# Performance work log

Hardware: AMD Instinct MI355X
Metric: run time of the kernel (lower is better)

Reference implementation:

```python
import jax, jax.numpy as jnp
import numpy as np

H = 16
D_MODEL = 1024
D_K = D_MODEL // H
NWORDS = 16384


def setup_inputs() -> dict:
    key0 = jax.random.key(0)
    ks = jax.random.split(key0, 11)
    s = 0.02
    return {
        "query": jax.random.normal(ks[0], (1, D_MODEL), dtype=jnp.float32),
        "key": jax.random.normal(ks[1], (NWORDS, D_MODEL), dtype=jnp.float32),
        "value": jax.random.normal(ks[2], (NWORDS, D_MODEL), dtype=jnp.float32),
        "Wq": jax.random.normal(ks[3], (D_MODEL, D_MODEL), dtype=jnp.float32) * s,
        "bq": jax.random.normal(ks[4], (D_MODEL,), dtype=jnp.float32) * s,
        "Wk": jax.random.normal(ks[5], (D_MODEL, D_MODEL), dtype=jnp.float32) * s,
        "bk": jax.random.normal(ks[6], (D_MODEL,), dtype=jnp.float32) * s,
        "Wv": jax.random.normal(ks[7], (D_MODEL, D_MODEL), dtype=jnp.float32) * s,
        "bv": jax.random.normal(ks[8], (D_MODEL,), dtype=jnp.float32) * s,
        "Wo": jax.random.normal(ks[9], (D_MODEL, D_MODEL), dtype=jnp.float32) * s,
        "bo": jax.random.normal(ks[10], (D_MODEL,), dtype=jnp.float32) * s,
    }


def reference(query, key, value, Wq, bq, Wk, bk, Wv, bv, Wo, bo):
    # torch Linear: y = x @ W.T + b
    q = (query @ Wq.T + bq).reshape(H, D_K)          # [h, d_k]  (single query token)
    k = (key @ Wk.T + bk).reshape(-1, H, D_K)        # [n, h, d_k]
    v = (value @ Wv.T + bv).reshape(-1, H, D_K)      # [n, h, d_k]
    # NOTE: original module applies NO 1/sqrt(d_k) scaling.
    scores = jnp.einsum("hd,nhd->hn", q, k)          # [h, n]
    p_attn = jax.nn.softmax(scores, axis=-1)          # dropout p=0 -> no-op
    x = jnp.einsum("hn,nhd->hd", p_attn, v).reshape(1, H * D_K)  # [1, d_model]
    return x @ Wo.T + bo                              # [1, d_model]
```

## Files before the change

kernel.cpp:

```cpp
#include <hip/hip_runtime.h>

#define DM 1024
#define NW 16384

#define OFF_C    1024
#define OFF_D0   17408
#define OFF_S    17424
#define OFF_X    17696
#define OFF_W    18720
#define OFF_E    36864
#define OFF_PART 299008

__global__ __launch_bounds__(256) void k_rowdot(const float* __restrict__ W,
                                                const float* __restrict__ v,
                                                const float* __restrict__ b,
                                                float* __restrict__ out) {
  const int wave = (blockIdx.x * 256 + threadIdx.x) >> 6;
  const int lane = threadIdx.x & 63;
  const float* row = W + (size_t)wave * DM + 4 * lane;
  float s = 0.f;
#pragma unroll
  for (int j = 0; j < 4; ++j) {
    float4 a = *(const float4*)(row + j * 256);
    float4 x = *(const float4*)(v + j * 256 + 4 * lane);
    s += a.x * x.x + a.y * x.y + a.z * x.z + a.w * x.w;
  }
#pragma unroll
  for (int off = 32; off; off >>= 1) s += __shfl_xor(s, off, 64);
  if (lane == 0) out[wave] = s + b[wave];
}

__global__ __launch_bounds__(256) void k_qck(const float* __restrict__ Wq,
                                             const float* __restrict__ bq,
                                             const float* __restrict__ query,
                                             const float* __restrict__ Wk,
                                             const float* __restrict__ bk,
                                             float* __restrict__ c,
                                             float* __restrict__ d0,
                                             float* __restrict__ S) {
  const int h = blockIdx.x >> 2;
  const int mc = blockIdx.x & 3;
  const int t = threadIdx.x;
  const int lane = t & 63;
  const int wv = t >> 6;
  __shared__ float qh[64];
  if (blockIdx.x == 0 && t < 16) S[t * 16] = 0.f;
  float4 qv[4];
#pragma unroll
  for (int j = 0; j < 4; ++j) qv[j] = *(const float4*)(query + j * 256 + 4 * lane);
#pragma unroll 1
  for (int i = 0; i < 16; i += 2) {
    const int d0i = 4 * i + wv;
    const int d1i = 4 * (i + 1) + wv;
    const float* r0 = Wq + (size_t)(h * 64 + d0i) * DM + 4 * lane;
    const float* r1 = Wq + (size_t)(h * 64 + d1i) * DM + 4 * lane;
    float4 a0[4], a1[4];
#pragma unroll
    for (int j = 0; j < 4; ++j) { a0[j] = *(const float4*)(r0 + j * 256);
                                  a1[j] = *(const float4*)(r1 + j * 256); }
    float s0 = 0.f, s1 = 0.f;
#pragma unroll
    for (int j = 0; j < 4; ++j) {
      s0 += a0[j].x * qv[j].x + a0[j].y * qv[j].y + a0[j].z * qv[j].z + a0[j].w * qv[j].w;
      s1 += a1[j].x * qv[j].x + a1[j].y * qv[j].y + a1[j].z * qv[j].z + a1[j].w * qv[j].w;
    }
#pragma unroll
    for (int off = 32; off; off >>= 1) { s0 += __shfl_xor(s0, off, 64);
                                         s1 += __shfl_xor(s1, off, 64); }
    if (lane == 0) { qh[d0i] = s0 + bq[h * 64 + d0i];
                     qh[d1i] = s1 + bq[h * 64 + d1i]; }
  }
  __syncthreads();
  const int m = mc * 256 + t;
  const float* Wp = Wk + (size_t)(h * 64) * DM + m;
  float s = 0.f;
#pragma unroll 1
  for (int db = 0; db < 8; ++db) {
    float wv8[8];
#pragma unroll
    for (int j = 0; j < 8; ++j) wv8[j] = Wp[(size_t)(db * 8 + j) * DM];
#pragma unroll
    for (int j = 0; j < 8; ++j) s = fmaf(qh[db * 8 + j], wv8[j], s);
  }
  c[h * DM + m] = s;
  if (mc == 0 && t == 0) {
    float tt = 0.f;
    for (int d = 0; d < 64; ++d) tt += qh[d] * bk[h * 64 + d];
    d0[h] = tt;
  }
}

__global__ __launch_bounds__(256, 3) void k_scores(const float* __restrict__ key,
                                                   const float* __restrict__ c,
                                                   const float* __restrict__ d0,
                                                   float* __restrict__ e,
                                                   float* __restrict__ S) {
  const int lane = threadIdx.x & 63;
  const int wv = threadIdx.x >> 6;
  const int hbase = wv * 4;
  const int n0 = blockIdx.x * 16;
  float4 cf[4][4];
#pragma unroll
  for (int hh = 0; hh < 4; ++hh)
#pragma unroll
    for (int j = 0; j < 4; ++j)
      cf[hh][j] = *(const float4*)(c + (size_t)(hbase + hh) * DM + j * 256 + 4 * lane);
  const int hl = (lane >> 4) & 3;
  const float dh = d0[hbase + hl];
  const bool hi5 = (lane & 32) != 0;
  const bool hi4 = (lane & 16) != 0;
  const bool writer = (lane & 15) == 0;
  float Ssum = 0.f;
  const float* kbase = key + (size_t)n0 * DM + 4 * lane;
  float4 kb[2][4];
#pragma unroll
  for (int j = 0; j < 4; ++j) {
    kb[0][j] = *(const float4*)(kbase + j * 256);
    kb[1][j] = *(const float4*)(kbase + DM + j * 256);
  }
#pragma unroll
  for (int rr = 0; rr < 8; ++rr) {
    float4 kn[2][4];
    if (rr < 7) {
      const float* kp = kbase + (size_t)(2 * rr + 2) * DM;
#pragma unroll
      for (int j = 0; j < 4; ++j) {
        kn[0][j] = *(const float4*)(kp + j * 256);
        kn[1][j] = *(const float4*)(kp + DM + j * 256);
      }
    }
#pragma unroll
    for (int b = 0; b < 2; ++b) {
      const int n = n0 + 2 * rr + b;
      float s[4];
#pragma unroll
      for (int hh = 0; hh < 4; ++hh) {
        s[hh] = cf[hh][0].x * kb[b][0].x + cf[hh][0].y * kb[b][0].y + cf[hh][0].z * kb[b][0].z + cf[hh][0].w * kb[b][0].w
              + cf[hh][1].x * kb[b][1].x + cf[hh][1].y * kb[b][1].y + cf[hh][1].z * kb[b][1].z + cf[hh][1].w * kb[b][1].w
              + cf[hh][2].x * kb[b][2].x + cf[hh][2].y * kb[b][2].y + cf[hh][2].z * kb[b][2].z + cf[hh][2].w * kb[b][2].w
              + cf[hh][3].x * kb[b][3].x + cf[hh][3].y * kb[b][3].y + cf[hh][3].z * kb[b][3].z + cf[hh][3].w * kb[b][3].w;
      }
      float keep0 = hi5 ? s[2] : s[0], send0 = hi5 ? s[0] : s[2];
      float v0 = keep0 + __shfl_xor(send0, 32, 64);
      float keep1 = hi5 ? s[3] : s[1], send1 = hi5 ? s[1] : s[3];
      float v1 = keep1 + __shfl_xor(send1, 32, 64);
      float keep = hi4 ? v1 : v0, send = hi4 ? v0 : v1;
      float t = keep + __shfl_xor(send, 16, 64);
      t += __shfl_xor(t, 8, 64);
      t += __shfl_xor(t, 4, 64);
      t += __shfl_xor(t, 2, 64);
      t += __shfl_xor(t, 1, 64);
      t = __expf(t + dh);
      if (writer) {
        e[(size_t)n * 16 + hbase + hl] = t;
        Ssum += t;
      }
    }
#pragma unroll
    for (int b = 0; b < 2; ++b)
#pragma unroll
      for (int j = 0; j < 4; ++j) kb[b][j] = kn[b][j];
  }
  if (writer) atomicAdd(S + (size_t)(hbase + hl) * 16, Ssum);
}

__global__ __launch_bounds__(256, 2) void k_pv(const float* __restrict__ value,
                                               const float* __restrict__ e,
                                               float* __restrict__ part) {
  const int nb = blockIdx.x >> 2;
  const int mc = blockIdx.x & 3;
  const int t = threadIdx.x;
  const int lane = t & 63;
  const int wy = t >> 6;
  const int col = mc * 256 + lane * 4;
  const int n0 = nb * 128;
  __shared__ float el[128 * 16];
  __shared__ float4 red[2][16][64];
  {
    const float4* eg = (const float4*)(e + (size_t)n0 * 16);
    float4* es = (float4*)el;
    es[t] = eg[t];
    es[t + 256] = eg[t + 256];
  }
  __syncthreads();
  float4 acc[16];
#pragma unroll
  for (int h = 0; h < 16; ++h) acc[h] = make_float4(0.f, 0.f, 0.f, 0.f);
  const float* vp = value + (size_t)(n0 + wy * 32) * DM + col;
  const float* ep = &el[wy * 32 * 16];
#pragma unroll 1
  for (int rb = 0; rb < 4; ++rb) {
    float4 v[8];
#pragma unroll
    for (int i = 0; i < 8; ++i) v[i] = *(const float4*)(vp + (size_t)(rb * 8 + i) * DM);
#pragma unroll
    for (int i = 0; i < 8; ++i) {
      const float4* er4 = (const float4*)(ep + (rb * 8 + i) * 16);
      float4 e0 = er4[0], e1 = er4[1], e2 = er4[2], e3 = er4[3];
      float4 vv = v[i];
#define FMA4H(H, P) { acc[H].x = fmaf(P, vv.x, acc[H].x); acc[H].y = fmaf(P, vv.y, acc[H].y); \
                      acc[H].z = fmaf(P, vv.z, acc[H].z); acc[H].w = fmaf(P, vv.w, acc[H].w); }
      FMA4H(0,  e0.x) FMA4H(1,  e0.y) FMA4H(2,  e0.z) FMA4H(3,  e0.w)
      FMA4H(4,  e1.x) FMA4H(5,  e1.y) FMA4H(6,  e1.z) FMA4H(7,  e1.w)
      FMA4H(8,  e2.x) FMA4H(9,  e2.y) FMA4H(10, e2.z) FMA4H(11, e2.w)
      FMA4H(12, e3.x) FMA4H(13, e3.y) FMA4H(14, e3.z) FMA4H(15, e3.w)
#undef FMA4H
    }
  }
  if (wy >= 2) {
#pragma unroll
    for (int h = 0; h < 16; ++h) red[wy - 2][h][lane] = acc[h];
  }
  __syncthreads();
  if (wy < 2) {
#pragma unroll
    for (int h = 0; h < 16; ++h) {
      float4 o = red[wy][h][lane];
      acc[h].x += o.x; acc[h].y += o.y; acc[h].z += o.z; acc[h].w += o.w;
    }
  }
  __syncthreads();
  if (wy == 1) {
#pragma unroll
    for (int h = 0; h < 16; ++h) red[0][h][lane] = acc[h];
  }
  __syncthreads();
  if (wy == 0) {
    float* pp = part + (size_t)nb * (16 * DM) + col;
#pragma unroll
    for (int h = 0; h < 16; ++h) {
      float4 o = red[0][h][lane];
      acc[h].x += o.x; acc[h].y += o.y; acc[h].z += o.z; acc[h].w += o.w;
      *(float4*)(pp + (size_t)h * DM) = acc[h];
    }
  }
}

__global__ __launch_bounds__(256) void k_wred(const float* __restrict__ part,
                                              float* __restrict__ w) {
  const int gid = blockIdx.x * 256 + threadIdx.x;
  const int o = gid >> 2;
  const int q = gid & 3;
  float s = 0.f;
#pragma unroll 1
  for (int ib = 0; ib < 4; ++ib) {
    float x[8];
#pragma unroll
    for (int j = 0; j < 8; ++j) x[j] = part[(size_t)(q * 32 + ib * 8 + j) * 16384 + o];
#pragma unroll
    for (int j = 0; j < 8; ++j) s += x[j];
  }
  s += __shfl_xor(s, 1, 64);
  s += __shfl_xor(s, 2, 64);
  if (q == 0) w[o] = s;
}

__global__ __launch_bounds__(256) void k_xproj(const float* __restrict__ Wv,
                                               const float* __restrict__ w,
                                               const float* __restrict__ bv,
                                               const float* __restrict__ S,
                                               float* __restrict__ x) {
  const int wave = (blockIdx.x * 256 + threadIdx.x) >> 6;
  const int lane = threadIdx.x & 63;
  const int h = wave >> 6;
  const float* vec = w + (size_t)h * DM;
  const float* row = Wv + (size_t)wave * DM + 4 * lane;
  float s = 0.f;
#pragma unroll
  for (int j = 0; j < 4; ++j) {
    float4 a = *(const float4*)(row + j * 256);
    float4 x4 = *(const float4*)(vec + j * 256 + 4 * lane);
    s += a.x * x4.x + a.y * x4.y + a.z * x4.z + a.w * x4.w;
  }
#pragma unroll
  for (int off = 32; off; off >>= 1) s += __shfl_xor(s, off, 64);
  if (lane == 0) x[wave] = s / S[(size_t)h * 16] + bv[wave];
}

extern "C" void kernel_launch(void* const* d_in, const int* in_sizes, int n_in,
                              void* d_out, int out_size, void* d_ws, size_t ws_size,
                              hipStream_t stream) {
  const float* query = (const float*)d_in[0];
  const float* key   = (const float*)d_in[1];
  const float* value = (const float*)d_in[2];
  const float* Wq    = (const float*)d_in[3];
  const float* bq    = (const float*)d_in[4];
  const float* Wk    = (const float*)d_in[5];
  const float* bk    = (const float*)d_in[6];
  const float* Wv    = (const float*)d_in[7];
  const float* bv    = (const float*)d_in[8];
  const float* Wo    = (const float*)d_in[9];
  const float* bo    = (const float*)d_in[10];
  float* out = (float*)d_out;
  float* ws  = (float*)d_ws;

  k_qck    <<<64,  256, 0, stream>>>(Wq, bq, query, Wk, bk, ws + OFF_C, ws + OFF_D0, ws + OFF_S);
  k_scores <<<1024,256, 0, stream>>>(key, ws + OFF_C, ws + OFF_D0, ws + OFF_E, ws + OFF_S);
  k_pv     <<<512, 256, 0, stream>>>(value, ws + OFF_E, ws + OFF_PART);
  k_wred   <<<256, 256, 0, stream>>>(ws + OFF_PART, ws + OFF_W);
  k_xproj  <<<256, 256, 0, stream>>>(Wv, ws + OFF_W, bv, ws + OFF_S, ws + OFF_X);
  k_rowdot <<<256, 256, 0, stream>>>(Wo, ws + OFF_X, bo, out);
}
```

Before: 240.3 us.

## Compute key scores with split-bf16 MFMA and double k_pv rows per block

The score kernel now runs on MFMA 16x16x32 bf16 instructions. Both the folded query-key vector and each key row are split into high and low bf16 parts, and three MFMAs are accumulated to get near-fp32 accuracy. The query-side matrix is pre-split and stored in an MFMA-friendly layout by k_qck, then staged in LDS. k_pv now handles 256 rows per block instead of 128, which halves the partial buffers that k_wred reduces. The risks are the extra conversion ALU work on every key element, 64KB of LDS per block limiting occupancy, and fewer blocks in k_pv.

```diff
diff --git a/kernel.cpp b/kernel.cpp
--- a/kernel.cpp
+++ b/kernel.cpp
@@ -3,13 +3,22 @@
 #define DM 1024
 #define NW 16384
 
-#define OFF_C    1024
+typedef __attribute__((ext_vector_type(8))) short short8;
+typedef __attribute__((ext_vector_type(4))) float f32x4;
+
+#define OFF_AH   1024
+#define OFF_AL   9216
 #define OFF_D0   17408
 #define OFF_S    17424
 #define OFF_X    17696
 #define OFF_W    18720
 #define OFF_E    36864
 #define OFF_PART 299008
+
+__device__ __forceinline__ unsigned short f2bf(float f) {
+  unsigned int u = __float_as_uint(f);
+  return (unsigned short)((u + 0x7fffu + ((u >> 16) & 1u)) >> 16);
+}
 
 __global__ __launch_bounds__(256) void k_rowdot(const float* __restrict__ W,
                                                 const float* __restrict__ v,
@@ -35,7 +44,8 @@
                                              const float* __restrict__ query,
                                              const float* __restrict__ Wk,
                                              const float* __restrict__ bk,
-                                             float* __restrict__ c,
+                                             short* __restrict__ Ah,
+                                             short* __restrict__ Al,
                                              float* __restrict__ d0,
                                              float* __restrict__ S) {
   const int h = blockIdx.x >> 2;
@@ -82,7 +92,13 @@
 #pragma unroll
     for (int j = 0; j < 8; ++j) s = fmaf(qh[db * 8 + j], wv8[j], s);
   }
-  c[h * DM + m] = s;
+  unsigned short hu = f2bf(s);
+  float hf = __uint_as_float(((unsigned int)hu) << 16);
+  unsigned short lu = f2bf(s - hf);
+  const int kb = m >> 5, q = (m >> 3) & 3, j = m & 7;
+  const int idx = (kb * 64 + q * 16 + h) * 8 + j;
+  Ah[idx] = (short)hu;
+  Al[idx] = (short)lu;
   if (mc == 0 && t == 0) {
     float tt = 0.f;
     for (int d = 0; d < 64; ++d) tt += qh[d] * bk[h * 64 + d];
@@ -90,78 +106,75 @@
   }
 }
 
-__global__ __launch_bounds__(256, 3) void k_scores(const float* __restrict__ key,
-                                                   const float* __restrict__ c,
-                                                   const float* __restrict__ d0,
-                                                   float* __restrict__ e,
-                                                   float* __restrict__ S) {
-  const int lane = threadIdx.x & 63;
-  const int wv = threadIdx.x >> 6;
-  const int hbase = wv * 4;
-  const int n0 = blockIdx.x * 16;
-  float4 cf[4][4];
-#pragma unroll
-  for (int hh = 0; hh < 4; ++hh)
-#pragma unroll
-    for (int j = 0; j < 4; ++j)
-      cf[hh][j] = *(const float4*)(c + (size_t)(hbase + hh) * DM + j * 256 + 4 * lane);
-  const int hl = (lane >> 4) & 3;
-  const float dh = d0[hbase + hl];
-  const bool hi5 = (lane & 32) != 0;
-  const bool hi4 = (lane & 16) != 0;
-  const bool writer = (lane & 15) == 0;
-  float Ssum = 0.f;
-  const float* kbase = key + (size_t)n0 * DM + 4 * lane;
-  float4 kb[2][4];
-#pragma unroll
-  for (int j = 0; j < 4; ++j) {
-    kb[0][j] = *(const float4*)(kbase + j * 256);
-    kb[1][j] = *(const float4*)(kbase + DM + j * 256);
-  }
-#pragma unroll
-  for (int rr = 0; rr < 8; ++rr) {
-    float4 kn[2][4];
-    if (rr < 7) {
-      const float* kp = kbase + (size_t)(2 * rr + 2) * DM;
-#pragma unroll
-      for (int j = 0; j < 4; ++j) {
-        kn[0][j] = *(const float4*)(kp + j * 256);
-        kn[1][j] = *(const float4*)(kp + DM + j * 256);
-      }
-    }
-#pragma unroll
-    for (int b = 0; b < 2; ++b) {
-      const int n = n0 + 2 * rr + b;
-      float s[4];
-#pragma unroll
-      for (int hh = 0; hh < 4; ++hh) {
-        s[hh] = cf[hh][0].x * kb[b][0].x + cf[hh][0].y * kb[b][0].y + cf[hh][0].z * kb[b][0].z + cf[hh][0].w * kb[b][0].w
-              + cf[hh][1].x * kb[b][1].x + cf[hh][1].y * kb[b][1].y + cf[hh][1].z * kb[b][1].z + cf[hh][1].w * kb[b][1].w
-              + cf[hh][2].x * kb[b][2].x + cf[hh][2].y * kb[b][2].y + cf[hh][2].z * kb[b][2].z + cf[hh][2].w * kb[b][2].w
-              + cf[hh][3].x * kb[b][3].x + cf[hh][3].y * kb[b][3].y + cf[hh][3].z * kb[b][3].z + cf[hh][3].w * kb[b][3].w;
-      }
-      float keep0 = hi5 ? s[2] : s[0], send0 = hi5 ? s[0] : s[2];
-      float v0 = keep0 + __shfl_xor(send0, 32, 64);
-      float keep1 = hi5 ? s[3] : s[1], send1 = hi5 ? s[1] : s[3];
-      float v1 = keep1 + __shfl_xor(send1, 32, 64);
-      float keep = hi4 ? v1 : v0, send = hi4 ? v0 : v1;
-      float t = keep + __shfl_xor(send, 16, 64);
-      t += __shfl_xor(t, 8, 64);
-      t += __shfl_xor(t, 4, 64);
-      t += __shfl_xor(t, 2, 64);
-      t += __shfl_xor(t, 1, 64);
-      t = __expf(t + dh);
-      if (writer) {
-        e[(size_t)n * 16 + hbase + hl] = t;
-        Ssum += t;
-      }
-    }
-#pragma unroll
-    for (int b = 0; b < 2; ++b)
-#pragma unroll
-      for (int j = 0; j < 4; ++j) kb[b][j] = kn[b][j];
-  }
-  if (writer) atomicAdd(S + (size_t)(hbase + hl) * 16, Ssum);
+__global__ __launch_bounds__(256) void k_scores(const float* __restrict__ key,
+                                                const short* __restrict__ AhG,
+                                                const short* __restrict__ AlG,
+                                                const float* __restrict__ d0,
+                                                float* __restrict__ e,
+                                                float* __restrict__ S) {
+  __shared__ short Ahi[16384];
+  __shared__ short Alo[16384];
+  const int t = threadIdx.x;
+  const int lane = t & 63;
+  const int wv = t >> 6;
+#pragma unroll
+  for (int i = 0; i < 8; ++i) {
+    *(short8*)&Ahi[(t + i * 256) * 8] = *(const short8*)&AhG[(t + i * 256) * 8];
+    *(short8*)&Alo[(t + i * 256) * 8] = *(const short8*)&AlG[(t + i * 256) * 8];
+  }
+  __syncthreads();
+
+  const int tile = blockIdx.x * 4 + wv;
+  const int n = tile * 16 + (lane & 15);
+  const int quad = lane >> 4;
+  const float* base = key + (size_t)n * DM + quad * 8;
+
+  f32x4 acc = {0.f, 0.f, 0.f, 0.f};
+  float4 f0[4], f1[4];
+#pragma unroll
+  for (int p = 0; p < 4; ++p) {
+    f0[p] = *(const float4*)(base + p * 32);
+    f1[p] = *(const float4*)(base + p * 32 + 4);
+  }
+#pragma unroll
+  for (int kb = 0; kb < 32; ++kb) {
+    const int slot = kb & 3;
+    float4 a0 = f0[slot], a1 = f1[slot];
+    if (kb < 28) {
+      f0[slot] = *(const float4*)(base + (kb + 4) * 32);
+      f1[slot] = *(const float4*)(base + (kb + 4) * 32 + 4);
+    }
+    short8 ah = *(const short8*)&Ahi[(kb * 64 + lane) * 8];
+    short8 al = *(const short8*)&Alo[(kb * 64 + lane) * 8];
+    float ff[8] = {a0.x, a0.y, a0.z, a0.w, a1.x, a1.y, a1.z, a1.w};
+    short8 bh, bl;
+#pragma unroll
+    for (int j = 0; j < 8; ++j) {
+      unsigned short hu = f2bf(ff[j]);
+      bh[j] = (short)hu;
+      float hf = __uint_as_float(((unsigned int)hu) << 16);
+      bl[j] = (short)f2bf(ff[j] - hf);
+    }
+    acc = __builtin_amdgcn_mfma_f32_16x16x32_bf16(ah, bh, acc, 0, 0, 0);
+    acc = __builtin_amdgcn_mfma_f32_16x16x32_bf16(ah, bl, acc, 0, 0, 0);
+    acc = __builtin_amdgcn_mfma_f32_16x16x32_bf16(al, bh, acc, 0, 0, 0);
+  }
+  const float4 dv = *(const float4*)(d0 + quad * 4);
+  float ex0 = __expf(acc[0] + dv.x);
+  float ex1 = __expf(acc[1] + dv.y);
+  float ex2 = __expf(acc[2] + dv.z);
+  float ex3 = __expf(acc[3] + dv.w);
+  *(float4*)(e + (size_t)n * 16 + quad * 4) = make_float4(ex0, ex1, ex2, ex3);
+  float sr[4] = {ex0, ex1, ex2, ex3};
+#pragma unroll
+  for (int r = 0; r < 4; ++r) {
+    float v = sr[r];
+    v += __shfl_xor(v, 1, 64);
+    v += __shfl_xor(v, 2, 64);
+    v += __shfl_xor(v, 4, 64);
+    v += __shfl_xor(v, 8, 64);
+    if ((lane & 15) == 0) atomicAdd(S + (size_t)(quad * 4 + r) * 16, v);
+  }
 }
 
 __global__ __launch_bounds__(256, 2) void k_pv(const float* __restrict__ value,
@@ -173,23 +186,23 @@
   const int lane = t & 63;
   const int wy = t >> 6;
   const int col = mc * 256 + lane * 4;
-  const int n0 = nb * 128;
-  __shared__ float el[128 * 16];
+  const int n0 = nb * 256;
+  __shared__ float el[256 * 16];
   __shared__ float4 red[2][16][64];
   {
     const float4* eg = (const float4*)(e + (size_t)n0 * 16);
     float4* es = (float4*)el;
-    es[t] = eg[t];
-    es[t + 256] = eg[t + 256];
+#pragma unroll
+    for (int k = 0; k < 4; ++k) es[t + k * 256] = eg[t + k * 256];
   }
   __syncthreads();
   float4 acc[16];
 #pragma unroll
   for (int h = 0; h < 16; ++h) acc[h] = make_float4(0.f, 0.f, 0.f, 0.f);
-  const float* vp = value + (size_t)(n0 + wy * 32) * DM + col;
-  const float* ep = &el[wy * 32 * 16];
+  const float* vp = value + (size_t)(n0 + wy * 64) * DM + col;
+  const float* ep = &el[wy * 64 * 16];
 #pragma unroll 1
-  for (int rb = 0; rb < 4; ++rb) {
+  for (int rb = 0; rb < 8; ++rb) {
     float4 v[8];
 #pragma unroll
     for (int i = 0; i < 8; ++i) v[i] = *(const float4*)(vp + (size_t)(rb * 8 + i) * DM);
@@ -243,10 +256,10 @@
   const int q = gid & 3;
   float s = 0.f;
 #pragma unroll 1
-  for (int ib = 0; ib < 4; ++ib) {
+  for (int ib = 0; ib < 2; ++ib) {
     float x[8];
 #pragma unroll
-    for (int j = 0; j < 8; ++j) x[j] = part[(size_t)(q * 32 + ib * 8 + j) * 16384 + o];
+    for (int j = 0; j < 8; ++j) x[j] = part[(size_t)(q * 16 + ib * 8 + j) * 16384 + o];
 #pragma unroll
     for (int j = 0; j < 8; ++j) s += x[j];
   }
@@ -293,10 +306,12 @@
   const float* bo    = (const float*)d_in[10];
   float* out = (float*)d_out;
   float* ws  = (float*)d_ws;
-
-  k_qck    <<<64,  256, 0, stream>>>(Wq, bq, query, Wk, bk, ws + OFF_C, ws + OFF_D0, ws + OFF_S);
-  k_scores <<<1024,256, 0, stream>>>(key, ws + OFF_C, ws + OFF_D0, ws + OFF_E, ws + OFF_S);
-  k_pv     <<<512, 256, 0, stream>>>(value, ws + OFF_E, ws + OFF_PART);
+  short* Ah  = (short*)(ws + OFF_AH);
+  short* Al  = (short*)(ws + OFF_AL);
+
+  k_qck    <<<64,  256, 0, stream>>>(Wq, bq, query, Wk, bk, Ah, Al, ws + OFF_D0, ws + OFF_S);
+  k_scores <<<256, 256, 0, stream>>>(key, Ah, Al, ws + OFF_D0, ws + OFF_E, ws + OFF_S);
+  k_pv     <<<256, 256, 0, stream>>>(value, ws + OFF_E, ws + OFF_PART);
   k_wred   <<<256, 256, 0, stream>>>(ws + OFF_PART, ws + OFF_W);
   k_xproj  <<<256, 256, 0, stream>>>(Wv, ws + OFF_W, bv, ws + OFF_S, ws + OFF_X);
   k_rowdot <<<256, 256, 0, stream>>>(Wo, ws + OFF_X, bo, out);
```

Result: no change. 240.8 us (+0.2%).
